# Performance work log

Hardware: AMD Instinct MI355X
Metric: run time of the kernel (lower is better)

Reference implementation:

```python
import jax, jax.numpy as jnp
import numpy as np

N_NODES = 100000
N_EDGES = 1600000
IN_DIM, HID, OUT = 6, 64, 32


def _linear_params(key, fan_in, fan_out):
    k1, k2 = jax.random.split(key)
    bound = 1.0 / np.sqrt(fan_in)
    W = jax.random.uniform(k1, (fan_in, fan_out), jnp.float32, -bound, bound)
    b = jax.random.uniform(k2, (fan_out,), jnp.float32, -bound, bound)
    return W, b


def setup_inputs() -> dict:
    key = jax.random.key(0)
    ks = jax.random.split(key, 9)
    x = jax.random.normal(ks[0], (N_NODES, IN_DIM), jnp.float32)
    edge_index = jax.random.randint(ks[1], (2, N_EDGES), 0, N_NODES, jnp.int64)
    edge_attr = jax.random.normal(ks[2], (N_EDGES, 3), jnp.float32)
    W1a, b1a = _linear_params(ks[3], IN_DIM + 3, HID)
    W1b, b1b = _linear_params(ks[4], HID, HID)
    W2a, b2a = _linear_params(ks[5], HID + 3, HID)
    W2b, b2b = _linear_params(ks[6], HID, HID)
    W3a, b3a = _linear_params(ks[7], HID + 3, OUT)
    W3b, b3b = _linear_params(ks[8], OUT, OUT)
    return {
        "x": x, "edge_index": edge_index, "edge_attr": edge_attr,
        "W1a": W1a, "b1a": b1a, "W1b": W1b, "b1b": b1b,
        "W2a": W2a, "b2a": b2a, "W2b": W2b, "b2b": b2b,
        "W3a": W3a, "b3a": b3a, "W3b": W3b, "b3b": b3b,
    }


def _gnn_layer(x, src, dst, edge_attr, Wa, ba, Wb, bb):
    # message: per-edge 2-layer MLP on [x_j, edge_attr]
    msg = jnp.concatenate([x[src], edge_attr], axis=-1)       # [E, in+3]
    h = jax.nn.relu(msg @ Wa + ba) @ Wb + bb                   # [E, out]
    # aggr='mean': scatter-sum into target nodes, divide by in-degree
    s = jax.ops.segment_sum(h, dst, num_segments=N_NODES)     # [N, out]
    cnt = jax.ops.segment_sum(jnp.ones((src.shape[0],), x.dtype), dst,
                              num_segments=N_NODES)
    return s / jnp.maximum(cnt, 1.0)[:, None]


def reference(x, edge_index, edge_attr,
              W1a, b1a, W1b, b1b,
              W2a, b2a, W2b, b2b,
              W3a, b3a, W3b, b3b):
    src, dst = edge_index[0], edge_index[1]   # x_j = x[src], aggregate at dst
    h = _gnn_layer(x, src, dst, edge_attr, W1a, b1a, W1b, b1b)
    h = jax.nn.relu(h)
    h = _gnn_layer(h, src, dst, edge_attr, W2a, b2a, W2b, b2b)
    h = jax.nn.relu(h)
    out = _gnn_layer(h, src, dst, edge_attr, W3a, b3a, W3b, b3b)
    return out
```

## Files before the change

### kernel.cpp

```cpp
#include <hip/hip_runtime.h>
#include <hip/hip_fp16.h>

#define N_NODES 100000
#define N_EDGES 1600000

__global__ __launch_bounds__(256) void degree_kernel(const int* __restrict__ dst,
                                                     int* __restrict__ cnt, int E) {
    int i = blockIdx.x * blockDim.x + threadIdx.x;
    int stride = gridDim.x * blockDim.x;
    for (; i < E; i += stride) atomicAdd(&cnt[dst[i]], 1);
}

__global__ __launch_bounds__(256) void inv_kernel(const int* __restrict__ cnt,
                                                  float* __restrict__ inv, int N) {
    int i = blockIdx.x * blockDim.x + threadIdx.x;
    if (i < N) inv[i] = (cnt[i] > 0) ? (1.0f / (float)cnt[i]) : 0.0f;
}

__global__ __launch_bounds__(256) void block_sum_kernel(const int* __restrict__ cnt,
                                                        int* __restrict__ bsum, int N) {
    __shared__ int s[256];
    const int tid = threadIdx.x;
    const int i = blockIdx.x * 256 + tid;
    s[tid] = (i < N) ? cnt[i] : 0;
    __syncthreads();
#pragma unroll
    for (int d = 128; d > 0; d >>= 1) {
        if (tid < d) s[tid] += s[tid + d];
        __syncthreads();
    }
    if (tid == 0) bsum[blockIdx.x] = s[0];
}

__global__ __launch_bounds__(512) void scan_bsum_kernel(int* __restrict__ bsum, int NB) {
    __shared__ int s[512];
    const int tid = threadIdx.x;
    const int v = (tid < NB) ? bsum[tid] : 0;
    s[tid] = v;
    __syncthreads();
    for (int d = 1; d < 512; d <<= 1) {
        const int t = (tid >= d) ? s[tid - d] : 0;
        __syncthreads();
        s[tid] += t;
        __syncthreads();
    }
    if (tid < NB) bsum[tid] = s[tid] - v;
}

__global__ __launch_bounds__(256) void make_cursor_kernel(const int* __restrict__ cnt,
                                                          const int* __restrict__ bsum,
                                                          int* __restrict__ cursor, int N) {
    __shared__ int s[256];
    const int tid = threadIdx.x;
    const int i = blockIdx.x * 256 + tid;
    const int v = (i < N) ? cnt[i] : 0;
    s[tid] = v;
    __syncthreads();
    for (int d = 1; d < 256; d <<= 1) {
        const int t = (tid >= d) ? s[tid - d] : 0;
        __syncthreads();
        s[tid] += t;
        __syncthreads();
    }
    if (i < N) cursor[i] = bsum[blockIdx.x] + s[tid] - v;
}

__global__ __launch_bounds__(256) void scatter_pack_kernel(
    const int* __restrict__ src, const int* __restrict__ dst,
    const float* __restrict__ ea,
    int* __restrict__ cursor, float4* __restrict__ spf, int E) {
    const int range = blockIdx.x & 7;
    const int lo = range * (N_NODES / 8);
    const int hi = lo + (N_NODES / 8);
    int i = (blockIdx.x >> 3) * blockDim.x + threadIdx.x;
    const int stride = (gridDim.x >> 3) * blockDim.x;
    for (; i < E; i += stride) {
        const int d = dst[i];
        if (d >= lo && d < hi) {
            const int pos = atomicAdd(&cursor[d], 1);
            spf[pos] = make_float4(__int_as_float(src[i]),
                                   ea[3 * (size_t)i + 0],
                                   ea[3 * (size_t)i + 1],
                                   ea[3 * (size_t)i + 2]);
        }
    }
}

__global__ __launch_bounds__(256) void node_gemm6h(
    const float* __restrict__ x, const float* __restrict__ W,
    const float* __restrict__ bias, __half* __restrict__ out_, int N) {
    int n = blockIdx.x * blockDim.x + threadIdx.x;
    if (n >= N) return;
    const float* row = x + (size_t)n * 6;
    float v[6];
#pragma unroll
    for (int k = 0; k < 6; ++k) v[k] = row[k];
    __half2* orow = (__half2*)(out_ + (size_t)n * 64);
    for (int g = 0; g < 16; ++g) {
        float a0 = bias[4 * g + 0], a1 = bias[4 * g + 1];
        float a2 = bias[4 * g + 2], a3 = bias[4 * g + 3];
#pragma unroll
        for (int k = 0; k < 6; ++k) {
            const float m = v[k];
            const float* w = &W[k * 64 + 4 * g];
            a0 = fmaf(m, w[0], a0);
            a1 = fmaf(m, w[1], a1);
            a2 = fmaf(m, w[2], a2);
            a3 = fmaf(m, w[3], a3);
        }
        orow[2 * g]     = __floats2half2_rn(a0, a1);
        orow[2 * g + 1] = __floats2half2_rn(a2, a3);
    }
}

template <int DNEXT, bool OUTH>
__global__ __launch_bounds__(256) void fused_agg64(
    const __half* __restrict__ P,
    const float4* __restrict__ spf,
    const int* __restrict__ cursor, const int* __restrict__ cnt,
    const float* __restrict__ inv,
    const float* __restrict__ We,
    const float* __restrict__ Wb,
    const float* __restrict__ bb,
    const float* __restrict__ Wn,
    const float* __restrict__ bn,
    void* __restrict__ Poutv, int N) {
    const int lane = threadIdx.x & 63;
    const int w    = threadIdx.x >> 6;
    const int q    = lane >> 4;
    const int p    = lane & 15;
    const int n    = blockIdx.x * 4 + w;

    __shared__ __align__(16) float lrow[4][64];

    float we0[4], we1[4], we2[4];
#pragma unroll
    for (int k = 0; k < 4; ++k) {
        we0[k] = We[0 * 64 + 4 * p + k];
        we1[k] = We[1 * 64 + 4 * p + k];
        we2[k] = We[2 * 64 + 4 * p + k];
    }

    const int end   = cursor[n];
    const int count = cnt[n];
    int j = end - count;
    const float s_inv = inv[n];
    const float mask  = (s_inv != 0.0f) ? 1.0f : 0.0f;

    float s0 = 0.f, s1 = 0.f, s2 = 0.f, s3 = 0.f;

#define GRP4H(base)                                                              \
    {                                                                            \
        const float4 f = spf[(base) + q];                                        \
        const ushort4 raw = *(const ushort4*)((const unsigned short*)P +         \
                            ((size_t)__float_as_int(f.x) << 6) + 4 * p);         \
        const float p0 = __half2float(__ushort_as_half(raw.x));                  \
        const float p1 = __half2float(__ushort_as_half(raw.y));                  \
        const float p2 = __half2float(__ushort_as_half(raw.z));                  \
        const float p3 = __half2float(__ushort_as_half(raw.w));                  \
        s0 += fmaxf(fmaf(f.w, we2[0], fmaf(f.z, we1[0], fmaf(f.y, we0[0], p0))), 0.f); \
        s1 += fmaxf(fmaf(f.w, we2[1], fmaf(f.z, we1[1], fmaf(f.y, we0[1], p1))), 0.f); \
        s2 += fmaxf(fmaf(f.w, we2[2], fmaf(f.z, we1[2], fmaf(f.y, we0[2], p2))), 0.f); \
        s3 += fmaxf(fmaf(f.w, we2[3], fmaf(f.z, we1[3], fmaf(f.y, we0[3], p3))), 0.f); \
    }

    for (; j + 8 <= end; j += 8) { GRP4H(j) GRP4H(j + 4) }
    if (j + 4 <= end) { GRP4H(j) j += 4; }
    const int rem = end - j;
    if (q < rem) { GRP4H(j) }
#undef GRP4H

    s0 += __shfl_xor(s0, 16); s1 += __shfl_xor(s1, 16);
    s2 += __shfl_xor(s2, 16); s3 += __shfl_xor(s3, 16);
    s0 += __shfl_xor(s0, 32); s1 += __shfl_xor(s1, 32);
    s2 += __shfl_xor(s2, 32); s3 += __shfl_xor(s3, 32);

    if (lane < 16) {
        *(float4*)&lrow[w][4 * p] =
            make_float4(s0 * s_inv, s1 * s_inv, s2 * s_inv, s3 * s_inv);
    }
    __builtin_amdgcn_wave_barrier();

    float m = bb[lane] * mask;
#pragma unroll
    for (int k = 0; k < 16; ++k) {
        const float4 r = *(const float4*)&lrow[w][4 * k];
        m = fmaf(r.x, Wb[(4 * k + 0) * 64 + lane], m);
        m = fmaf(r.y, Wb[(4 * k + 1) * 64 + lane], m);
        m = fmaf(r.z, Wb[(4 * k + 2) * 64 + lane], m);
        m = fmaf(r.w, Wb[(4 * k + 3) * 64 + lane], m);
    }
    m = fmaxf(m, 0.0f);
    __builtin_amdgcn_wave_barrier();
    lrow[w][lane] = m;
    __builtin_amdgcn_wave_barrier();
    const int c2 = lane % DNEXT;
    float o = bn[c2];
#pragma unroll
    for (int k = 0; k < 16; ++k) {
        const float4 r = *(const float4*)&lrow[w][4 * k];
        o = fmaf(r.x, Wn[(4 * k + 0) * DNEXT + c2], o);
        o = fmaf(r.y, Wn[(4 * k + 1) * DNEXT + c2], o);
        o = fmaf(r.z, Wn[(4 * k + 2) * DNEXT + c2], o);
        o = fmaf(r.w, Wn[(4 * k + 3) * DNEXT + c2], o);
    }
    if (lane < DNEXT) {
        if constexpr (OUTH)
            ((__half*)Poutv)[(size_t)n * DNEXT + lane] = __float2half_rn(o);
        else
            ((float*)Poutv)[(size_t)n * DNEXT + lane] = o;
    }
}

__global__ __launch_bounds__(256) void fused_agg32(
    const float* __restrict__ P,
    const float4* __restrict__ spf,
    const int* __restrict__ cursor, const int* __restrict__ cnt,
    const float* __restrict__ inv,
    const float* __restrict__ We,
    const float* __restrict__ Wb,
    const float* __restrict__ bb,
    float* __restrict__ out, int N) {
    const int lane = threadIdx.x & 63;
    const int w    = threadIdx.x >> 6;
    const int q    = lane >> 4;
    const int p    = lane & 15;
    const int n    = blockIdx.x * 4 + w;

    __shared__ __align__(16) float lrow[4][32];

    float we0[2], we1[2], we2[2];
#pragma unroll
    for (int k = 0; k < 2; ++k) {
        we0[k] = We[0 * 32 + 2 * p + k];
        we1[k] = We[1 * 32 + 2 * p + k];
        we2[k] = We[2 * 32 + 2 * p + k];
    }

    const int end   = cursor[n];
    const int count = cnt[n];
    int j = end - count;
    const float s_inv = inv[n];
    const float mask  = (s_inv != 0.0f) ? 1.0f : 0.0f;

    float s0 = 0.f, s1 = 0.f;

#define GRP4F(base)                                                              \
    {                                                                            \
        const float4 f = spf[(base) + q];                                        \
        const float2 pr = *(const float2*)(P +                                   \
                          ((size_t)__float_as_int(f.x) << 5) + 2 * p);           \
        s0 += fmaxf(fmaf(f.w, we2[0], fmaf(f.z, we1[0], fmaf(f.y, we0[0], pr.x))), 0.f); \
        s1 += fmaxf(fmaf(f.w, we2[1], fmaf(f.z, we1[1], fmaf(f.y, we0[1], pr.y))), 0.f); \
    }

    for (; j + 8 <= end; j += 8) { GRP4F(j) GRP4F(j + 4) }
    if (j + 4 <= end) { GRP4F(j) j += 4; }
    const int rem = end - j;
    if (q < rem) { GRP4F(j) }
#undef GRP4F

    s0 += __shfl_xor(s0, 16); s1 += __shfl_xor(s1, 16);
    s0 += __shfl_xor(s0, 32); s1 += __shfl_xor(s1, 32);

    if (lane < 16) {
        *(float2*)&lrow[w][2 * p] = make_float2(s0 * s_inv, s1 * s_inv);
    }
    __builtin_amdgcn_wave_barrier();

    const int c = lane & 31;
    float m = bb[c] * mask;
#pragma unroll
    for (int k = 0; k < 8; ++k) {
        const float4 r = *(const float4*)&lrow[w][4 * k];
        m = fmaf(r.x, Wb[(4 * k + 0) * 32 + c], m);
        m = fmaf(r.y, Wb[(4 * k + 1) * 32 + c], m);
        m = fmaf(r.z, Wb[(4 * k + 2) * 32 + c], m);
        m = fmaf(r.w, Wb[(4 * k + 3) * 32 + c], m);
    }
    if (lane < 32) out[(size_t)n * 32 + c] = m;
}

extern "C" void kernel_launch(void* const* d_in, const int* in_sizes, int n_in,
                              void* d_out, int out_size, void* d_ws, size_t ws_size,
                              hipStream_t stream) {
    const float* x   = (const float*)d_in[0];
    const int*   ei  = (const int*)d_in[1];
    const float* ea  = (const float*)d_in[2];
    const float* W1a = (const float*)d_in[3];
    const float* b1a = (const float*)d_in[4];
    const float* W1b = (const float*)d_in[5];
    const float* b1b = (const float*)d_in[6];
    const float* W2a = (const float*)d_in[7];
    const float* b2a = (const float*)d_in[8];
    const float* W2b = (const float*)d_in[9];
    const float* b2b = (const float*)d_in[10];
    const float* W3a = (const float*)d_in[11];
    const float* b3a = (const float*)d_in[12];
    const float* W3b = (const float*)d_in[13];
    const float* b3b = (const float*)d_in[14];

    const int* src = ei;
    const int* dst = ei + N_EDGES;
    float* out = (float*)d_out;

    char* ws = (char*)d_ws;
    int*    cnt    = (int*)(ws);
    float*  inv    = (float*)(ws + 0x80000);
    int*    bsum   = (int*)(ws + 0x100000);
    int*    cursor = (int*)(ws + 0x110000);
    float4* spf    = (float4*)(ws + 0x200000);
    __half* PH1    = (__half*)(ws + 0x1B00000);
    __half* PH2    = (__half*)(ws + 0x2800000);
    float*  P3     = (float*)(ws + 0x3500000);

    const int NBLK = (N_NODES + 255) / 256;

    hipMemsetAsync(cnt, 0, N_NODES * sizeof(int), stream);
    degree_kernel<<<2048, 256, 0, stream>>>(dst, cnt, N_EDGES);
    inv_kernel<<<NBLK, 256, 0, stream>>>(cnt, inv, N_NODES);
    block_sum_kernel<<<NBLK, 256, 0, stream>>>(cnt, bsum, N_NODES);
    scan_bsum_kernel<<<1, 512, 0, stream>>>(bsum, NBLK);
    make_cursor_kernel<<<NBLK, 256, 0, stream>>>(cnt, bsum, cursor, N_NODES);
    scatter_pack_kernel<<<2048, 256, 0, stream>>>(src, dst, ea, cursor, spf, N_EDGES);

    node_gemm6h<<<NBLK, 256, 0, stream>>>(x, W1a, b1a, PH1, N_NODES);

    fused_agg64<64, true><<<N_NODES / 4, 256, 0, stream>>>(
        PH1, spf, cursor, cnt, inv, W1a + 6 * 64, W1b, b1b, W2a, b2a, PH2, N_NODES);
    fused_agg64<32, false><<<N_NODES / 4, 256, 0, stream>>>(
        PH2, spf, cursor, cnt, inv, W2a + 64 * 64, W2b, b2b, W3a, b3a, P3, N_NODES);
    fused_agg32<<<N_NODES / 4, 256, 0, stream>>>(
        P3, spf, cursor, cnt, inv, W3a + 64 * 32, W3b, b3b, out, N_NODES);
}
```

Baseline: 490.1 us.

## Partition degree atomics by node range, prefetch edge records, store layer-3 projections in fp16

The degree kernel now splits blocks into eight node-range groups. Each block scans the edge list and issues atomics only for destinations in its range, which is meant to cut atomic contention and improve locality at the cost of reading dst eight times. The aggregation loops are restructured to software-prefetch the next group of packed edge records, using clamped indices and a validity mask in place of the separate remainder paths. The layer-3 node projection is now stored in half precision and gathered as half2, halving gather traffic at some cost in accuracy.

```diff
diff --git a/kernel.cpp b/kernel.cpp
--- a/kernel.cpp
+++ b/kernel.cpp
@@ -6,9 +6,15 @@
 
 __global__ __launch_bounds__(256) void degree_kernel(const int* __restrict__ dst,
                                                      int* __restrict__ cnt, int E) {
-    int i = blockIdx.x * blockDim.x + threadIdx.x;
-    int stride = gridDim.x * blockDim.x;
-    for (; i < E; i += stride) atomicAdd(&cnt[dst[i]], 1);
+    const int range = blockIdx.x & 7;
+    const int lo = range * (N_NODES / 8);
+    const int hi = lo + (N_NODES / 8);
+    int i = (blockIdx.x >> 3) * blockDim.x + threadIdx.x;
+    const int stride = (gridDim.x >> 3) * blockDim.x;
+    for (; i < E; i += stride) {
+        const int d = dst[i];
+        if (d >= lo && d < hi) atomicAdd(&cnt[d], 1);
+    }
 }
 
 __global__ __launch_bounds__(256) void inv_kernel(const int* __restrict__ cnt,
@@ -149,26 +155,37 @@
 
     float s0 = 0.f, s1 = 0.f, s2 = 0.f, s3 = 0.f;
 
-#define GRP4H(base)                                                              \
+#define PROC64(f, valid)                                                         \
     {                                                                            \
-        const float4 f = spf[(base) + q];                                        \
         const ushort4 raw = *(const ushort4*)((const unsigned short*)P +         \
-                            ((size_t)__float_as_int(f.x) << 6) + 4 * p);         \
+                            ((size_t)__float_as_int((f).x) << 6) + 4 * p);       \
         const float p0 = __half2float(__ushort_as_half(raw.x));                  \
         const float p1 = __half2float(__ushort_as_half(raw.y));                  \
         const float p2 = __half2float(__ushort_as_half(raw.z));                  \
         const float p3 = __half2float(__ushort_as_half(raw.w));                  \
-        s0 += fmaxf(fmaf(f.w, we2[0], fmaf(f.z, we1[0], fmaf(f.y, we0[0], p0))), 0.f); \
-        s1 += fmaxf(fmaf(f.w, we2[1], fmaf(f.z, we1[1], fmaf(f.y, we0[1], p1))), 0.f); \
-        s2 += fmaxf(fmaf(f.w, we2[2], fmaf(f.z, we1[2], fmaf(f.y, we0[2], p2))), 0.f); \
-        s3 += fmaxf(fmaf(f.w, we2[3], fmaf(f.z, we1[3], fmaf(f.y, we0[3], p3))), 0.f); \
-    }
-
-    for (; j + 8 <= end; j += 8) { GRP4H(j) GRP4H(j + 4) }
-    if (j + 4 <= end) { GRP4H(j) j += 4; }
-    const int rem = end - j;
-    if (q < rem) { GRP4H(j) }
-#undef GRP4H
+        const float h0 = fmaxf(fmaf((f).w, we2[0], fmaf((f).z, we1[0], fmaf((f).y, we0[0], p0))), 0.f); \
+        const float h1 = fmaxf(fmaf((f).w, we2[1], fmaf((f).z, we1[1], fmaf((f).y, we0[1], p1))), 0.f); \
+        const float h2 = fmaxf(fmaf((f).w, we2[2], fmaf((f).z, we1[2], fmaf((f).y, we0[2], p2))), 0.f); \
+        const float h3 = fmaxf(fmaf((f).w, we2[3], fmaf((f).z, we1[3], fmaf((f).y, we0[3], p3))), 0.f); \
+        if (valid) { s0 += h0; s1 += h1; s2 += h2; s3 += h3; }                   \
+    }
+
+    if (count > 0) {
+        const int e0 = j + q,     e1 = j + 4 + q;
+        float4 f0 = spf[e0 < end ? e0 : end - 1];
+        float4 f1 = spf[e1 < end ? e1 : end - 1];
+        while (j + 8 < end) {
+            const int g0i = j + 8 + q, g1i = j + 12 + q;
+            const float4 g0 = spf[g0i < end ? g0i : end - 1];
+            const float4 g1 = spf[g1i < end ? g1i : end - 1];
+            PROC64(f0, true)
+            PROC64(f1, true)
+            f0 = g0; f1 = g1; j += 8;
+        }
+        PROC64(f0, (j + q < end))
+        PROC64(f1, (j + 4 + q < end))
+    }
+#undef PROC64
 
     s0 += __shfl_xor(s0, 16); s1 += __shfl_xor(s1, 16);
     s2 += __shfl_xor(s2, 16); s3 += __shfl_xor(s3, 16);
@@ -212,8 +229,8 @@
     }
 }
 
-__global__ __launch_bounds__(256) void fused_agg32(
-    const float* __restrict__ P,
+__global__ __launch_bounds__(256) void fused_agg32h(
+    const __half* __restrict__ P,
     const float4* __restrict__ spf,
     const int* __restrict__ cursor, const int* __restrict__ cnt,
     const float* __restrict__ inv,
@@ -245,20 +262,32 @@
 
     float s0 = 0.f, s1 = 0.f;
 
-#define GRP4F(base)                                                              \
+#define PROC32(f, valid)                                                         \
     {                                                                            \
-        const float4 f = spf[(base) + q];                                        \
-        const float2 pr = *(const float2*)(P +                                   \
-                          ((size_t)__float_as_int(f.x) << 5) + 2 * p);           \
-        s0 += fmaxf(fmaf(f.w, we2[0], fmaf(f.z, we1[0], fmaf(f.y, we0[0], pr.x))), 0.f); \
-        s1 += fmaxf(fmaf(f.w, we2[1], fmaf(f.z, we1[1], fmaf(f.y, we0[1], pr.y))), 0.f); \
-    }
-
-    for (; j + 8 <= end; j += 8) { GRP4F(j) GRP4F(j + 4) }
-    if (j + 4 <= end) { GRP4F(j) j += 4; }
-    const int rem = end - j;
-    if (q < rem) { GRP4F(j) }
-#undef GRP4F
+        const __half2 pr = *(const __half2*)((const __half*)P +                  \
+                           ((size_t)__float_as_int((f).x) << 5) + 2 * p);        \
+        const float2 pf = __half22float2(pr);                                    \
+        const float h0 = fmaxf(fmaf((f).w, we2[0], fmaf((f).z, we1[0], fmaf((f).y, we0[0], pf.x))), 0.f); \
+        const float h1 = fmaxf(fmaf((f).w, we2[1], fmaf((f).z, we1[1], fmaf((f).y, we0[1], pf.y))), 0.f); \
+        if (valid) { s0 += h0; s1 += h1; }                                       \
+    }
+
+    if (count > 0) {
+        const int e0 = j + q,     e1 = j + 4 + q;
+        float4 f0 = spf[e0 < end ? e0 : end - 1];
+        float4 f1 = spf[e1 < end ? e1 : end - 1];
+        while (j + 8 < end) {
+            const int g0i = j + 8 + q, g1i = j + 12 + q;
+            const float4 g0 = spf[g0i < end ? g0i : end - 1];
+            const float4 g1 = spf[g1i < end ? g1i : end - 1];
+            PROC32(f0, true)
+            PROC32(f1, true)
+            f0 = g0; f1 = g1; j += 8;
+        }
+        PROC32(f0, (j + q < end))
+        PROC32(f1, (j + 4 + q < end))
+    }
+#undef PROC32
 
     s0 += __shfl_xor(s0, 16); s1 += __shfl_xor(s1, 16);
     s0 += __shfl_xor(s0, 32); s1 += __shfl_xor(s1, 32);
@@ -312,7 +341,7 @@
     float4* spf    = (float4*)(ws + 0x200000);
     __half* PH1    = (__half*)(ws + 0x1B00000);
     __half* PH2    = (__half*)(ws + 0x2800000);
-    float*  P3     = (float*)(ws + 0x3500000);
+    __half* P3h    = (__half*)(ws + 0x3500000);
 
     const int NBLK = (N_NODES + 255) / 256;
 
@@ -328,8 +357,8 @@
 
     fused_agg64<64, true><<<N_NODES / 4, 256, 0, stream>>>(
         PH1, spf, cursor, cnt, inv, W1a + 6 * 64, W1b, b1b, W2a, b2a, PH2, N_NODES);
-    fused_agg64<32, false><<<N_NODES / 4, 256, 0, stream>>>(
-        PH2, spf, cursor, cnt, inv, W2a + 64 * 64, W2b, b2b, W3a, b3a, P3, N_NODES);
-    fused_agg32<<<N_NODES / 4, 256, 0, stream>>>(
-        P3, spf, cursor, cnt, inv, W3a + 64 * 32, W3b, b3b, out, N_NODES);
-}
+    fused_agg64<32, true><<<N_NODES / 4, 256, 0, stream>>>(
+        PH2, spf, cursor, cnt, inv, W2a + 64 * 64, W2b, b2b, W3a, b3a, P3h, N_NODES);
+    fused_agg32h<<<N_NODES / 4, 256, 0, stream>>>(
+        P3h, spf, cursor, cnt, inv, W3a + 64 * 32, W3b, b3b, out, N_NODES);
+}
```

New measurement: 483.8 us. No clear change (-1.3%).
